# Optimization experiments

Measured on AMD Instinct MI355X. Metric: run time of the kernel, lower is better.

Reference implementation:

```python
import jax, jax.numpy as jnp
import numpy as np

GROUPS = 32
GN_EPS = 1e-6


def setup_inputs() -> dict:
    key = jax.random.key(0)
    ks = jax.random.split(key, 6)
    B, C, H, W = 2, 512, 64, 64
    s = 1.0 / np.sqrt(C)
    return {
        "x": jax.random.normal(ks[0], (B, C, H, W), jnp.float32),
        "gamma": jnp.ones((C,), jnp.float32),
        "beta": jnp.zeros((C,), jnp.float32),
        "wq": jax.random.normal(ks[1], (C, C), jnp.float32) * s,
        "bq": jnp.zeros((C,), jnp.float32),
        "wk": jax.random.normal(ks[2], (C, C), jnp.float32) * s,
        "bk": jnp.zeros((C,), jnp.float32),
        "wv": jax.random.normal(ks[3], (C, C), jnp.float32) * s,
        "bv": jnp.zeros((C,), jnp.float32),
        "wp": jax.random.normal(ks[4], (C, C), jnp.float32) * s,
        "bp": jnp.zeros((C,), jnp.float32),
    }


def _group_norm(x, gamma, beta):
    B, C, H, W = x.shape
    xg = x.reshape(B, GROUPS, C // GROUPS, H, W)
    mean = jnp.mean(xg, axis=(2, 3, 4), keepdims=True)
    var = jnp.mean(jnp.square(xg - mean), axis=(2, 3, 4), keepdims=True)
    xn = ((xg - mean) * jax.lax.rsqrt(var + GN_EPS)).reshape(B, C, H, W)
    return xn * gamma[None, :, None, None] + beta[None, :, None, None]


def _conv1x1(x, w, b):
    # 1x1 conv == per-pixel linear over channels; w: [out, in]
    return jnp.einsum('oc,bchw->bohw', w, x) + b[None, :, None, None]


def reference(x, gamma, beta, wq, bq, wk, bk, wv, bv, wp, bp):
    B, C, H, W = x.shape
    N = H * W
    h = _group_norm(x, gamma, beta)
    q = _conv1x1(h, wq, bq).reshape(B, C, N)  # [B, C, N]
    k = _conv1x1(h, wk, bk).reshape(B, C, N)
    v = _conv1x1(h, wv, bv).reshape(B, C, N)
    scale = C ** (-0.5)
    # attn[b, i, j] = softmax_j(q_i . k_j * scale)
    scores = jnp.einsum('bci,bcj->bij', q, k) * scale
    attn = jax.nn.softmax(scores, axis=2)
    # out[b, c, i] = sum_j attn[b, i, j] * v[b, c, j]
    o = jnp.einsum('bij,bcj->bci', attn, v).reshape(B, C, H, W)
    o = _conv1x1(o, wp, bp)
    return x + o
```

## Files before the change

### kernel.cpp

```cpp
#include <hip/hip_runtime.h>
#include <hip/hip_bf16.h>

using bf16 = __hip_bfloat16;
typedef __attribute__((ext_vector_type(4))) float f32x4;
typedef __attribute__((ext_vector_type(8))) short bf16x8;

#define NPX 4096
#define CCH 512

struct Ptr8 { void* p[8]; };

struct GemmP {
  const bf16* A; const bf16* B; void* C;
  const float* bias_m; const float* bias_n; const float* resid;
  float* rspart;
  float alpha; int K;
  int lda, ldb, ldc;
  long long sA, sB, sC, sR;
  int gx, gy;
  int omode;
};

__device__ __forceinline__ void async16(const bf16* g, bf16* l) {
  __builtin_amdgcn_global_load_lds((const __attribute__((address_space(1))) void*)g,
                                   (__attribute__((address_space(3))) void*)l, 16, 0, 0);
}

__device__ __forceinline__ float bfb2f(short s) {
  unsigned u = ((unsigned)(unsigned short)s) << 16;
  float f;
  __builtin_memcpy(&f, &u, 4);
  return f;
}

__device__ __forceinline__ short f2bfb(float f) {
  bf16 h = __float2bfloat16(f);
  short s;
  __builtin_memcpy(&s, &h, 2);
  return s;
}

__global__ __launch_bounds__(256) void prep_kernel(
    const float* __restrict__ wq, const float* __restrict__ wk,
    const float* __restrict__ wv, const float* __restrict__ wp,
    const float* __restrict__ bq, const float* __restrict__ bk,
    const float* __restrict__ x,
    bf16* __restrict__ wout, float* __restrict__ bqk, float* __restrict__ pstats) {
  int bid = blockIdx.x;
  int t = threadIdx.x;
  if (bid < 1024) {
    int tid = bid * 256 + t;
    int i = tid * 4;
    int seg = i >> 18;
    const float* in = seg == 0 ? wq : seg == 1 ? wk : seg == 2 ? wv : wp;
    float4 v = *reinterpret_cast<const float4*>(in + (i & 262143));
    wout[i]     = __float2bfloat16(v.x);
    wout[i + 1] = __float2bfloat16(v.y);
    wout[i + 2] = __float2bfloat16(v.z);
    wout[i + 3] = __float2bfloat16(v.w);
    if (tid < 256) {
      int j = tid * 4;
      const float* bsrc = j < 512 ? bq : bk;
      float4 b = *reinterpret_cast<const float4*>(bsrc + (j & 511));
      *reinterpret_cast<float4*>(bqk + j) = b;
    }
  } else {
    int bp = bid - 1024;
    const float* p = x + (size_t)bp * 8192;
    float s = 0.f, s2 = 0.f;
    #pragma unroll
    for (int j = 0; j < 8; j++) {
      float4 v = *reinterpret_cast<const float4*>(p + j * 1024 + t * 4);
      s  += v.x + v.y + v.z + v.w;
      s2 += v.x * v.x + v.y * v.y + v.z * v.z + v.w * v.w;
    }
    #pragma unroll
    for (int off = 32; off >= 1; off >>= 1) {
      s  += __shfl_xor(s, off);
      s2 += __shfl_xor(s2, off);
    }
    __shared__ float ls[8];
    int wv_ = t >> 6;
    if ((t & 63) == 0) { ls[wv_ * 2] = s; ls[wv_ * 2 + 1] = s2; }
    __syncthreads();
    if (t == 0) {
      pstats[bp * 2]     = ls[0] + ls[2] + ls[4] + ls[6];
      pstats[bp * 2 + 1] = ls[1] + ls[3] + ls[5] + ls[7];
    }
  }
}

__global__ __launch_bounds__(256) void gn_apply_kernel(const float* __restrict__ x,
    const float* __restrict__ pstats, const float* __restrict__ gamma,
    const float* __restrict__ beta, bf16* __restrict__ h) {
  __shared__ float tile[64][65];
  __shared__ float mr[4][2];
  int b  = blockIdx.z;
  int c0 = blockIdx.x * 64, n0 = blockIdx.y * 64;
  int t  = threadIdx.x;
  if (t < 4) {
    int g = (c0 >> 4) + t;
    float S = 0.f, S2 = 0.f;
    #pragma unroll
    for (int k2 = 0; k2 < 8; k2++) {
      S  += pstats[((b * 32 + g) * 8 + k2) * 2];
      S2 += pstats[((b * 32 + g) * 8 + k2) * 2 + 1];
    }
    float mean = S * (1.f / 65536.f);
    float var  = S2 * (1.f / 65536.f) - mean * mean;
    mr[t][0] = mean;
    mr[t][1] = rsqrtf(var + 1e-6f);
  }
  __syncthreads();
  int cl = t >> 6, nl = t & 63;
  #pragma unroll
  for (int i = 0; i < 16; i++) {
    int c = c0 + cl + i * 4;
    float v = x[((size_t)b * CCH + c) * NPX + n0 + nl];
    int gi = (cl + i * 4) >> 4;
    tile[cl + i * 4][nl] = (v - mr[gi][0]) * mr[gi][1] * gamma[c] + beta[c];
  }
  __syncthreads();
  #pragma unroll
  for (int i = 0; i < 16; i++) {
    int n = cl + i * 4;
    int c = nl;
    h[((size_t)b * NPX + n0 + n) * CCH + c0 + c] = __float2bfloat16(tile[c][n]);
  }
}

__global__ __launch_bounds__(256, 4) void gemm_any_kernel(GemmP p0, GemmP p1, unsigned nb0) {
  unsigned nwg = gridDim.x;
  unsigned flat = blockIdx.x;
  unsigned swz = (flat & 7) * (nwg >> 3) + (flat >> 3);
  GemmP p = swz < nb0 ? p0 : p1;
  unsigned local = swz < nb0 ? swz : swz - nb0;
  unsigned bxi = local % p.gx;
  unsigned tmp = local / p.gx;
  unsigned byi = tmp % p.gy;
  unsigned bz  = tmp / p.gy;

  const bf16* A = p.A + (size_t)bz * p.sA;
  const bf16* B = p.B + (size_t)bz * p.sB;
  const int m0 = bxi * 128, n0 = byi * 128;

  __shared__ bf16 ldsA[128 * 64];
  __shared__ bf16 ldsB[128 * 64];

  const int t = threadIdx.x;
  const int lane = t & 63, wv = t >> 6;
  const int wr = (wv >> 1) * 64, wc = (wv & 1) * 64;

  const int r0 = t >> 3;
  const int cb = ((t & 7) << 4) ^ ((r0 & 7) << 4);
  const bf16* gA = A + (size_t)(m0 + r0) * p.lda + (cb >> 1);
  const bf16* gB = B + (size_t)(n0 + r0) * p.ldb + (cb >> 1);
  bf16* lA = ldsA + t * 8;
  bf16* lB = ldsB + t * 8;

  const int arow = wr + (lane & 15);
  const int brow = wc + (lane & 15);
  const int kb   = (lane >> 4) * 16;

  f32x4 acc[4][4] = {};

  for (int k0 = 0; k0 < p.K; k0 += 64) {
    #pragma unroll
    for (int i = 0; i < 4; i++) {
      async16(gA + (size_t)i * 32 * p.lda + k0, lA + i * 2048);
      async16(gB + (size_t)i * 32 * p.ldb + k0, lB + i * 2048);
    }
    __syncthreads();
    #pragma unroll
    for (int ks = 0; ks < 2; ks++) {
      bf16x8 af[4], bfr[4];
      #pragma unroll
      for (int f = 0; f < 4; f++) {
        int ra = arow + f * 16;
        af[f] = *reinterpret_cast<const bf16x8*>(
            reinterpret_cast<const char*>(ldsA) + ra * 128 + ((ks * 64 + kb) ^ ((ra & 7) << 4)));
        int rb = brow + f * 16;
        bfr[f] = *reinterpret_cast<const bf16x8*>(
            reinterpret_cast<const char*>(ldsB) + rb * 128 + ((ks * 64 + kb) ^ ((rb & 7) << 4)));
      }
      #pragma unroll
      for (int fm = 0; fm < 4; fm++)
        #pragma unroll
        for (int fn = 0; fn < 4; fn++)
          acc[fm][fn] = __builtin_amdgcn_mfma_f32_16x16x32_bf16(af[fm], bfr[fn], acc[fm][fn], 0, 0, 0);
    }
    __syncthreads();
  }

  #pragma unroll
  for (int fm = 0; fm < 4; fm++) {
    #pragma unroll
    for (int j = 0; j < 4; j++) {
      int gm = m0 + wr + fm * 16 + (lane >> 4) * 4 + j;
      if (p.omode == 2) {
        float rsum = 0.f;
        #pragma unroll
        for (int fn = 0; fn < 4; fn++) {
          int gn = n0 + wc + fn * 16 + (lane & 15);
          float e = __expf(acc[fm][fn][j] * p.alpha);
          rsum += e;
          reinterpret_cast<bf16*>(p.C)[(size_t)bz * p.sC + (size_t)gm * p.ldc + gn] = __float2bfloat16(e);
        }
        rsum += __shfl_xor(rsum, 1);
        rsum += __shfl_xor(rsum, 2);
        rsum += __shfl_xor(rsum, 4);
        rsum += __shfl_xor(rsum, 8);
        if ((lane & 15) == 0)
          p.rspart[(((size_t)bz * 4096 + gm) << 6) + byi * 2 + (wv & 1)] = rsum;
      } else {
        float bm = p.bias_m ? p.bias_m[gm] : 0.f;
        #pragma unroll
        for (int fn = 0; fn < 4; fn++) {
          int gn = n0 + wc + fn * 16 + (lane & 15);
          float vv = acc[fm][fn][j] * p.alpha + bm;
          if (p.bias_n) vv += p.bias_n[gn];
          if (p.resid)  vv += p.resid[(size_t)bz * p.sR + (size_t)gm * p.ldc + gn];
          if (p.omode == 1)
            reinterpret_cast<bf16*>(p.C)[(size_t)bz * p.sC + (size_t)gm * p.ldc + gn] = __float2bfloat16(vv);
          else
            reinterpret_cast<float*>(p.C)[(size_t)bz * p.sC + (size_t)gm * p.ldc + gn] = vv;
        }
      }
    }
  }
}

#define BAR() __builtin_amdgcn_s_barrier()
#define LGKM0() do { asm volatile("s_waitcnt lgkmcnt(0)" ::: "memory"); \
                     __builtin_amdgcn_sched_barrier(0); } while (0)
#define VMC2() do { asm volatile("s_waitcnt vmcnt(2)" ::: "memory"); \
                    __builtin_amdgcn_sched_barrier(0); } while (0)
#define VMC0() do { asm volatile("s_waitcnt vmcnt(0)" ::: "memory"); \
                    __builtin_amdgcn_sched_barrier(0); } while (0)

#define STG(op, buf, half, kt, LD) do { \
    const bf16* _s = (op ? gB : gA) + (size_t)((half) * 128) * (LD) + (kt) * 64; \
    bf16* _d = &lds[op][buf][half][t * 8]; \
    async16(_s, _d); \
    async16(_s + (size_t)64 * (LD), _d + 4096); \
  } while (0)

#define DSA(buf, mrb) do { \
    _Pragma("unroll") \
    for (int mi = 0; mi < 4; mi++) { \
      int _r = ((mrb) + mi) * 16 + (l & 15); \
      _Pragma("unroll") \
      for (int ks = 0; ks < 2; ks++) \
        aR[mi][ks] = *reinterpret_cast<const bf16x8*>( \
            &lds[0][buf][wm][_r * 64 + ((ks * 32 + (l >> 4) * 8) ^ ((l & 7) << 3))]); \
    } } while (0)

#define DSB(buf, nrb) do { \
    _Pragma("unroll") \
    for (int ni = 0; ni < 2; ni++) { \
      int _r = (wn & 1) * 64 + ((nrb) + ni) * 16 + (l & 15); \
      _Pragma("unroll") \
      for (int ks = 0; ks < 2; ks++) \
        bR[ni][ks] = *reinterpret_cast<const bf16x8*>( \
            &lds[1][buf][wn >> 1][_r * 64 + ((ks * 32 + (l >> 4) * 8) ^ ((l & 7) << 3))]); \
    } } while (0)

#define MMAQ(qm, qn) do { \
    _Pragma("unroll") \
    for (int mi = 0; mi < 4; mi++) \
    _Pragma("unroll") \
    for (int ni = 0; ni < 2; ni++) \
    _Pragma("unroll") \
    for (int ks = 0; ks < 2; ks++) \
      acc[(qm) * 4 + mi][(qn) * 2 + ni] = __builtin_amdgcn_mfma_f32_16x16x32_bf16( \
          aR[mi][ks], bR[ni][ks], acc[(qm) * 4 + mi][(qn) * 2 + ni], 0, 0, 0); \
  } while (0)

#define PH_TAIL(qm, qn) do { \
    BAR(); LGKM0(); \
    __builtin_amdgcn_s_setprio(1); MMAQ(qm, qn); __builtin_amdgcn_s_setprio(0); \
    BAR(); } while (0)

__global__ __launch_bounds__(512, 1) void pv8_kernel(
    const bf16* __restrict__ Sb, const bf16* __restrict__ vb,
    const float* __restrict__ rspart, Ptr8 slots) {
  unsigned nwg = gridDim.x;
  unsigned flat = blockIdx.x;
  unsigned swz = (flat & 7) * (nwg >> 3) + (flat >> 3);
  const unsigned zz = swz >> 5;
  const unsigned tile = swz & 31;
  const int m0 = (tile & 15) * 256;
  const int n0 = (tile >> 4) * 256;
  const int b = zz >> 2, s = zz & 3;
  const bf16* A = Sb + (size_t)b * 16777216 + s * 1024;
  const bf16* B = vb + (size_t)b * 2097152 + s * 1024;
  bf16* Cp = (bf16*)(slots.p[zz]);

  __shared__ bf16 lds[2][2][2][8192];
  __shared__ float rs_lds[256];

  const int t = threadIdx.x;
  const int l = t & 63;
  const int wid = t >> 6;
  const int wm = wid >> 2;
  const int wn = wid & 3;

  const int swzc = (((t & 7) ^ ((t >> 3) & 7)) << 3);
  const bf16* gA = A + (size_t)(m0 + (t >> 3)) * 4096 + swzc;
  const bf16* gB = B + (size_t)(n0 + (t >> 3)) * 4096 + swzc;

  f32x4 acc[8][4] = {};
  bf16x8 aR[4][2], bR[2][2];

  STG(0, 0, 0, 0, 4096);
  STG(0, 0, 1, 0, 4096);
  STG(1, 0, 0, 0, 4096);
  STG(1, 0, 1, 0, 4096);
  STG(1, 1, 0, 1, 4096);
  VMC0();
  BAR();

  #pragma unroll 1
  for (int j = 0; j < 7; j++) {
    const int kt1 = 2 * j + 1, kt2 = 2 * j + 2, kt3 = 2 * j + 3;
    DSA(0, 0); DSB(0, 0); STG(1, 1, 1, kt1, 4096); PH_TAIL(0, 0);
    DSA(0, 4);            STG(0, 1, 0, kt1, 4096); PH_TAIL(1, 0);
    DSB(0, 2);            STG(0, 1, 1, kt1, 4096); PH_TAIL(1, 1);
    DSA(0, 0);            STG(1, 0, 0, kt2, 4096); VMC2(); PH_TAIL(0, 1);
    DSA(1, 0); DSB(1, 0); STG(1, 0, 1, kt2, 4096); PH_TAIL(0, 0);
    DSA(1, 4);            STG(0, 0, 0, kt2, 4096); PH_TAIL(1, 0);
    DSB(1, 2);            STG(0, 0, 1, kt2, 4096); PH_TAIL(1, 1);
    DSA(1, 0);            STG(1, 1, 0, kt3, 4096); VMC2(); PH_TAIL(0, 1);
  }
  {
    const int kt1 = 15;
    DSA(0, 0); DSB(0, 0); STG(1, 1, 1, kt1, 4096); PH_TAIL(0, 0);
    DSA(0, 4);            STG(0, 1, 0, kt1, 4096); PH_TAIL(1, 0);
    DSB(0, 2);            STG(0, 1, 1, kt1, 4096); PH_TAIL(1, 1);
    DSA(0, 0);            VMC0(); PH_TAIL(0, 1);
    DSA(1, 0); DSB(1, 0); PH_TAIL(0, 0);
    DSA(1, 4);            PH_TAIL(1, 0);
    DSB(1, 2);            PH_TAIL(1, 1);
    DSA(1, 0);            PH_TAIL(0, 1);
  }

  if (t < 256) {
    const float4* pp = reinterpret_cast<const float4*>(
        rspart + (((size_t)b * 4096 + m0 + t) << 6));
    float ssum = 0.f;
    #pragma unroll
    for (int i2 = 0; i2 < 16; i2++) {
      float4 vv = pp[i2];
      ssum += vv.x + vv.y + vv.z + vv.w;
    }
    rs_lds[t] = 1.0f / ssum;
  }
  __syncthreads();

  #pragma unroll
  for (int mr = 0; mr < 8; mr++) {
    #pragma unroll
    for (int jj = 0; jj < 4; jj++) {
      int lrow = wm * 128 + mr * 16 + (l >> 4) * 4 + jj;
      float inv = rs_lds[lrow];
      int gm = m0 + lrow;
      #pragma unroll
      for (int nr = 0; nr < 4; nr++) {
        int gn = n0 + wn * 64 + nr * 16 + (l & 15);
        Cp[(size_t)gm * 512 + gn] = __float2bfloat16(acc[mr][nr][jj] * inv);
      }
    }
  }
}

__global__ __launch_bounds__(512, 1) void qk8_kernel(
    const bf16* __restrict__ qkb, bf16* __restrict__ Sb,
    float* __restrict__ rspart, float scale) {
  unsigned nwg = gridDim.x;
  unsigned flat = blockIdx.x;
  unsigned swz = (flat & 7) * (nwg >> 3) + (flat >> 3);
  const unsigned b = swz >> 8;
  const unsigned tile = swz & 255;
  const int m0 = (tile & 15) * 256;
  const int n0 = (tile >> 4) * 256;
  const bf16* A = qkb + (size_t)b * 4194304;
  const bf16* B = qkb + (size_t)b * 4194304 + 512;
  bf16* Cp = Sb + (size_t)b * 16777216;

  __shared__ bf16 lds[2][2][2][8192];

  const int t = threadIdx.x;
  const int l = t & 63;
  const int wid = t >> 6;
  const int wm = wid >> 2;
  const int wn = wid & 3;

  const int swzc = (((t & 7) ^ ((t >> 3) & 7)) << 3);
  const bf16* gA = A + (size_t)(m0 + (t >> 3)) * 1024 + swzc;
  const bf16* gB = B + (size_t)(n0 + (t >> 3)) * 1024 + swzc;

  f32x4 acc[8][4] = {};
  bf16x8 aR[4][2], bR[2][2];

  STG(0, 0, 0, 0, 1024);
  STG(0, 0, 1, 0, 1024);
  STG(1, 0, 0, 0, 1024);
  STG(1, 0, 1, 0, 1024);
  STG(1, 1, 0, 1, 1024);
  VMC0();
  BAR();

  #pragma unroll 1
  for (int j = 0; j < 3; j++) {
    const int kt1 = 2 * j + 1, kt2 = 2 * j + 2, kt3 = 2 * j + 3;
    DSA(0, 0); DSB(0, 0); STG(1, 1, 1, kt1, 1024); PH_TAIL(0, 0);
    DSA(0, 4);            STG(0, 1, 0, kt1, 1024); PH_TAIL(1, 0);
    DSB(0, 2);            STG(0, 1, 1, kt1, 1024); PH_TAIL(1, 1);
    DSA(0, 0);            STG(1, 0, 0, kt2, 1024); VMC2(); PH_TAIL(0, 1);
    DSA(1, 0); DSB(1, 0); STG(1, 0, 1, kt2, 1024); PH_TAIL(0, 0);
    DSA(1, 4);            STG(0, 0, 0, kt2, 1024); PH_TAIL(1, 0);
    DSB(1, 2);            STG(0, 0, 1, kt2, 1024); PH_TAIL(1, 1);
    DSA(1, 0);            STG(1, 1, 0, kt3, 1024); VMC2(); PH_TAIL(0, 1);
  }
  {
    const int kt1 = 7;
    DSA(0, 0); DSB(0, 0); STG(1, 1, 1, kt1, 1024); PH_TAIL(0, 0);
    DSA(0, 4);            STG(0, 1, 0, kt1, 1024); PH_TAIL(1, 0);
    DSB(0, 2);            STG(0, 1, 1, kt1, 1024); PH_TAIL(1, 1);
    DSA(0, 0);            VMC0(); PH_TAIL(0, 1);
    DSA(1, 0); DSB(1, 0); PH_TAIL(0, 0);
    DSA(1, 4);            PH_TAIL(1, 0);
    DSB(1, 2);            PH_TAIL(1, 1);
    DSA(1, 0);            PH_TAIL(0, 1);
  }

  const int ntile = tile >> 4;
  #pragma unroll
  for (int mr = 0; mr < 8; mr++) {
    #pragma unroll
    for (int jj = 0; jj < 4; jj++) {
      int gm = m0 + wm * 128 + mr * 16 + (l >> 4) * 4 + jj;
      float rsum = 0.f;
      #pragma unroll
      for (int nr = 0; nr < 4; nr++) {
        int gn = n0 + wn * 64 + nr * 16 + (l & 15);
        float e = __expf(acc[mr][nr][jj] * scale);
        rsum += e;
        Cp[(size_t)gm * 4096 + gn] = __float2bfloat16(e);
      }
      rsum += __shfl_xor(rsum, 1);
      rsum += __shfl_xor(rsum, 2);
      rsum += __shfl_xor(rsum, 4);
      rsum += __shfl_xor(rsum, 8);
      if ((l & 15) == 0)
        rspart[(((size_t)b * 4096 + gm) << 6) + ntile * 4 + wn] = rsum;
    }
  }
}

__global__ __launch_bounds__(256, 4) void pv_split_kernel(
    const bf16* __restrict__ Sb, const bf16* __restrict__ vb,
    const float* __restrict__ rspart,
    long long sS, long long sV, Ptr8 slots, int mode) {
  unsigned nx = gridDim.x, ny = gridDim.y;
  unsigned flat = (blockIdx.z * ny + blockIdx.y) * nx + blockIdx.x;
  unsigned nwg = nx * ny * gridDim.z;
  unsigned swz = (flat & 7) * (nwg >> 3) + (flat >> 3);
  unsigned bxi = swz % nx;
  unsigned tmp = swz / nx;
  unsigned byi = tmp % ny;
  unsigned bz  = tmp / ny;

  const int z = bz;
  const int b = mode ? 0 : (z >> 2);
  const int s = mode ? z : (z & 3);
  const bf16* A = Sb + (size_t)b * sS + s * 1024;
  const bf16* B = vb + (size_t)b * sV + s * 1024;
  bf16* Cp = (bf16*)(slots.p[z]);
  const int m0 = bxi * 128, n0 = byi * 128;

  __shared__ bf16 ldsA[128 * 64];
  __shared__ bf16 ldsB[128 * 64];
  __shared__ float rs_lds[128];

  const int t = threadIdx.x;

  if (t < 128) {
    const float4* pp = reinterpret_cast<const float4*>(rspart + (((size_t)b * 4096 + m0 + t) << 6));
    float ssum = 0.f;
    #pragma unroll
    for (int i2 = 0; i2 < 16; i2++) {
      float4 vv = pp[i2];
      ssum += vv.x + vv.y + vv.z + vv.w;
    }
    rs_lds[t] = 1.0f / ssum;
  }

  const int lane = t & 63, wv = t >> 6;
  const int wr = (wv >> 1) * 64, wc = (wv & 1) * 64;

  const int r0 = t >> 3;
  const int cb = ((t & 7) << 4) ^ ((r0 & 7) << 4);
  const bf16* gA = A + (size_t)(m0 + r0) * 4096 + (cb >> 1);
  const bf16* gB = B + (size_t)(n0 + r0) * 4096 + (cb >> 1);
  bf16* lA = ldsA + t * 8;
  bf16* lB = ldsB + t * 8;

  const int arow = wr + (lane & 15);
  const int brow = wc + (lane & 15);
  const int kb   = (lane >> 4) * 16;

  f32x4 acc[4][4] = {};

  for (int k0 = 0; k0 < 1024; k0 += 64) {
    #pragma unroll
    for (int i = 0; i < 4; i++) {
      async16(gA + (size_t)i * 32 * 4096 + k0, lA + i * 2048);
      async16(gB + (size_t)i * 32 * 4096 + k0, lB + i * 2048);
    }
    __syncthreads();
    #pragma unroll
    for (int ks = 0; ks < 2; ks++) {
      bf16x8 af[4], bfr[4];
      #pragma unroll
      for (int f = 0; f < 4; f++) {
        int ra = arow + f * 16;
        af[f] = *reinterpret_cast<const bf16x8*>(
            reinterpret_cast<const char*>(ldsA) + ra * 128 + ((ks * 64 + kb) ^ ((ra & 7) << 4)));
        int rb = brow + f * 16;
        bfr[f] = *reinterpret_cast<const bf16x8*>(
            reinterpret_cast<const char*>(ldsB) + rb * 128 + ((ks * 64 + kb) ^ ((rb & 7) << 4)));
      }
      #pragma unroll
      for (int fm = 0; fm < 4; fm++)
        #pragma unroll
        for (int fn = 0; fn < 4; fn++)
          acc[fm][fn] = __builtin_amdgcn_mfma_f32_16x16x32_bf16(af[fm], bfr[fn], acc[fm][fn], 0, 0, 0);
    }
    __syncthreads();
  }

  #pragma unroll
  for (int fm = 0; fm < 4; fm++) {
    #pragma unroll
    for (int j = 0; j < 4; j++) {
      int lrow = wr + fm * 16 + (lane >> 4) * 4 + j;
      float inv = rs_lds[lrow];
      int gm = m0 + lrow;
      #pragma unroll
      for (int fn = 0; fn < 4; fn++) {
        int gn = n0 + wc + fn * 16 + (lane & 15);
        Cp[(size_t)gm * 512 + gn] = __float2bfloat16(acc[fm][fn][j] * inv);
      }
    }
  }
}

__global__ __launch_bounds__(256) void reduce3x2_kernel(bf16* __restrict__ o,
    const bf16* __restrict__ h, const bf16* __restrict__ qk) {
  int i = (blockIdx.x * 256 + threadIdx.x) * 8;
  int b = i >> 21;
  int ii = i & 2097151;
  bf16* dst = o + (size_t)b * 2097152 + ii;
  const bf16* p1 = h + (size_t)b * 2097152 + ii;
  const bf16* p2 = qk + (size_t)b * 2 * 2097152 + ii;
  const bf16* p3 = qk + (size_t)(b * 2 + 1) * 2097152 + ii;
  bf16x8 a  = *reinterpret_cast<const bf16x8*>(dst);
  bf16x8 v1 = *reinterpret_cast<const bf16x8*>(p1);
  bf16x8 v2 = *reinterpret_cast<const bf16x8*>(p2);
  bf16x8 v3 = *reinterpret_cast<const bf16x8*>(p3);
  bf16x8 r;
  #pragma unroll
  for (int j = 0; j < 8; j++)
    r[j] = f2bfb(bfb2f(a[j]) + bfb2f(v1[j]) + bfb2f(v2[j]) + bfb2f(v3[j]));
  *reinterpret_cast<bf16x8*>(dst) = r;
}

__global__ __launch_bounds__(256) void reduce3_kernel(bf16* __restrict__ dst,
    const bf16* __restrict__ p1, const bf16* __restrict__ p2,
    const bf16* __restrict__ p3) {
  int i = (blockIdx.x * 256 + threadIdx.x) * 8;
  bf16x8 a  = *reinterpret_cast<const bf16x8*>(dst + i);
  bf16x8 v1 = *reinterpret_cast<const bf16x8*>(p1 + i);
  bf16x8 v2 = *reinterpret_cast<const bf16x8*>(p2 + i);
  bf16x8 v3 = *reinterpret_cast<const bf16x8*>(p3 + i);
  bf16x8 r;
  #pragma unroll
  for (int j = 0; j < 8; j++)
    r[j] = f2bfb(bfb2f(a[j]) + bfb2f(v1[j]) + bfb2f(v2[j]) + bfb2f(v3[j]));
  *reinterpret_cast<bf16x8*>(dst + i) = r;
}

extern "C" void kernel_launch(void* const* d_in, const int* in_sizes, int n_in,
                              void* d_out, int out_size, void* d_ws, size_t ws_size,
                              hipStream_t stream) {
  const float* x     = (const float*)d_in[0];
  const float* gamma = (const float*)d_in[1];
  const float* beta  = (const float*)d_in[2];
  const float* wq    = (const float*)d_in[3];
  const float* bq    = (const float*)d_in[4];
  const float* wk    = (const float*)d_in[5];
  const float* bk    = (const float*)d_in[6];
  const float* wv    = (const float*)d_in[7];
  const float* bv    = (const float*)d_in[8];
  const float* wp    = (const float*)d_in[9];
  const float* bp    = (const float*)d_in[10];
  float* out = (float*)d_out;

  char* w = (char*)d_ws;
  size_t off = 0;
  float* pstats = (float*)(w + off);   off += 4096;
  float* bqk    = (float*)(w + off);   off += 4096;
  float* rspart = (float*)(w + off);   off += (size_t)2 * 4096 * 64 * 4;
  bf16* wqkb = (bf16*)(w + off);       off += (size_t)1024 * 512 * 2;
  bf16* wvb  = (bf16*)(w + off);       off += (size_t)512 * 512 * 2;
  bf16* wpb  = (bf16*)(w + off);       off += (size_t)512 * 512 * 2;
  bf16* h    = (bf16*)(w + off);       off += (size_t)2 * NPX * CCH * 2;
  bf16* qk   = (bf16*)(w + off);       off += (size_t)2 * NPX * 1024 * 2;
  bf16* v    = (bf16*)(w + off);       off += (size_t)2 * NPX * CCH * 2;
  bf16* o    = (bf16*)(w + off);       off += (size_t)2 * NPX * CCH * 2;
  bf16* S    = (bf16*)(w + off);
  size_t need_big = off + (size_t)2 * NPX * NPX * 2;
  const bool big = ws_size >= need_big;

  const long long sBN = (long long)NPX * CCH;
  const long long sQK = (long long)NPX * 1024;
  const long long sS  = (long long)NPX * NPX;
  const float scale = 0.04419417382415922f;

  prep_kernel<<<1536, 256, 0, stream>>>(wq, wk, wv, wp, bq, bk, x, wqkb, bqk, pstats);
  gn_apply_kernel<<<dim3(8, 64, 2), 256, 0, stream>>>(x, pstats, gamma, beta, h);

  GemmP pqkv = {h, wqkb, qk, nullptr, bqk, nullptr, nullptr,
                1.f, 512, 512, 512, 1024, sBN, 0, sQK, 0, 32, 8, 1};
  GemmP pv   = {wvb, h, v, bv, nullptr, nullptr, nullptr,
                1.f, 512, 512, 512, 4096, 0, sBN, sBN, 0, 4, 32, 1};
  gemm_any_kernel<<<768, 256, 0, stream>>>(pqkv, pv, 512);

  if (big) {
    qk8_kernel<<<512, 512, 0, stream>>>(qk, S, rspart, scale);
    Ptr8 slots{{o, h, qk, qk + sBN, o + sBN, h + sBN, qk + 2 * sBN, qk + 3 * sBN}};
    pv8_kernel<<<256, 512, 0, stream>>>(S, v, rspart, slots);
    reduce3x2_kernel<<<2048, 256, 0, stream>>>(o, h, qk);
  } else {
    for (int b = 0; b < 2; b++) {
      GemmP ps = {qk + b * sQK, qk + b * sQK + 512, S, nullptr, nullptr, nullptr,
                  rspart + ((size_t)b << 18),
                  scale, 512, 1024, 1024, 4096, 0, 0, 0, 0, 32, 32, 2};
      gemm_any_kernel<<<1024, 256, 0, stream>>>(ps, ps, 1024);
      Ptr8 slots{{o + b * sBN, h, h + sBN, (bf16*)out, nullptr, nullptr, nullptr, nullptr}};
      pv_split_kernel<<<dim3(32, 4, 4), 256, 0, stream>>>(S, v + b * sBN,
          rspart + ((size_t)b << 18), 0, 0, slots, 1);
      reduce3_kernel<<<1024, 256, 0, stream>>>(o + b * sBN, h, h + sBN, (bf16*)out);
    }
  }

  GemmP po = {wpb, o, out, bp, nullptr, x, nullptr,
              1.f, 512, 512, 512, 4096, 0, sBN, sBN, sBN, 4, 32, 0};
  gemm_any_kernel<<<256, 256, 0, stream>>>(po, po, 256);
}
```

Baseline: 246.3 us.

## Process both batches per workgroup in QK kernel with mid-loop epilogue

```diff
diff --git a/kernel.cpp b/kernel.cpp
--- a/kernel.cpp
+++ b/kernel.cpp
@@ -220,7 +220,7 @@
           float vv = acc[fm][fn][j] * p.alpha + bm;
           if (p.bias_n) vv += p.bias_n[gn];
           if (p.resid)  vv += p.resid[(size_t)bz * p.sR + (size_t)gm * p.ldc + gn];
-          if (p.omode == 1)
+        if (p.omode == 1)
             reinterpret_cast<bf16*>(p.C)[(size_t)bz * p.sC + (size_t)gm * p.ldc + gn] = __float2bfloat16(vv);
           else
             reinterpret_cast<float*>(p.C)[(size_t)bz * p.sC + (size_t)gm * p.ldc + gn] = vv;
@@ -243,6 +243,15 @@
     bf16* _d = &lds[op][buf][half][t * 8]; \
     async16(_s, _d); \
     async16(_s + (size_t)64 * (LD), _d + 4096); \
+  } while (0)
+
+#define STGQ(op, buf, half, kt) do { \
+    int _k = (kt); \
+    const bf16* _base = (op) ? (_k < 8 ? gB0 : gB1) : (_k < 8 ? gA0 : gA1); \
+    const bf16* _s = _base + (size_t)((half) * 128) * 1024 + (_k & 7) * 64; \
+    bf16* _d = &lds[op][buf][half][t * 8]; \
+    async16(_s, _d); \
+    async16(_s + (size_t)64 * 1024, _d + 4096); \
   } while (0)
 
 #define DSA(buf, mrb) do { \
@@ -379,13 +388,9 @@
   unsigned nwg = gridDim.x;
   unsigned flat = blockIdx.x;
   unsigned swz = (flat & 7) * (nwg >> 3) + (flat >> 3);
-  const unsigned b = swz >> 8;
   const unsigned tile = swz & 255;
   const int m0 = (tile & 15) * 256;
   const int n0 = (tile >> 4) * 256;
-  const bf16* A = qkb + (size_t)b * 4194304;
-  const bf16* B = qkb + (size_t)b * 4194304 + 512;
-  bf16* Cp = Sb + (size_t)b * 16777216;
 
   __shared__ bf16 lds[2][2][2][8192];
 
@@ -396,66 +401,80 @@
   const int wn = wid & 3;
 
   const int swzc = (((t & 7) ^ ((t >> 3) & 7)) << 3);
-  const bf16* gA = A + (size_t)(m0 + (t >> 3)) * 1024 + swzc;
-  const bf16* gB = B + (size_t)(n0 + (t >> 3)) * 1024 + swzc;
+  const bf16* gA0 = qkb + (size_t)(m0 + (t >> 3)) * 1024 + swzc;
+  const bf16* gB0 = qkb + 512 + (size_t)(n0 + (t >> 3)) * 1024 + swzc;
+  const bf16* gA1 = gA0 + 4194304;
+  const bf16* gB1 = gB0 + 4194304;
 
   f32x4 acc[8][4] = {};
   bf16x8 aR[4][2], bR[2][2];
 
-  STG(0, 0, 0, 0, 1024);
-  STG(0, 0, 1, 0, 1024);
-  STG(1, 0, 0, 0, 1024);
-  STG(1, 0, 1, 0, 1024);
-  STG(1, 1, 0, 1, 1024);
+  auto epi = [&](int b) {
+    const int ntile = tile >> 4;
+    bf16* Cp = Sb + (size_t)b * 16777216;
+    #pragma unroll
+    for (int mr = 0; mr < 8; mr++) {
+      #pragma unroll
+      for (int jj = 0; jj < 4; jj++) {
+        int gm = m0 + wm * 128 + mr * 16 + (l >> 4) * 4 + jj;
+        float rsum = 0.f;
+        #pragma unroll
+        for (int nr = 0; nr < 4; nr++) {
+          int gn = n0 + wn * 64 + nr * 16 + (l & 15);
+          float e = __expf(acc[mr][nr][jj] * scale);
+          rsum += e;
+          Cp[(size_t)gm * 4096 + gn] = __float2bfloat16(e);
+        }
+        rsum += __shfl_xor(rsum, 1);
+        rsum += __shfl_xor(rsum, 2);
+        rsum += __shfl_xor(rsum, 4);
+        rsum += __shfl_xor(rsum, 8);
+        if ((l & 15) == 0)
+          rspart[(((size_t)b * 4096 + gm) << 6) + ntile * 4 + wn] = rsum;
+      }
+    }
+  };
+
+  STGQ(0, 0, 0, 0);
+  STGQ(0, 0, 1, 0);
+  STGQ(1, 0, 0, 0);
+  STGQ(1, 0, 1, 0);
+  STGQ(1, 1, 0, 1);
   VMC0();
   BAR();
 
   #pragma unroll 1
-  for (int j = 0; j < 3; j++) {
+  for (int j = 0; j < 7; j++) {
     const int kt1 = 2 * j + 1, kt2 = 2 * j + 2, kt3 = 2 * j + 3;
-    DSA(0, 0); DSB(0, 0); STG(1, 1, 1, kt1, 1024); PH_TAIL(0, 0);
-    DSA(0, 4);            STG(0, 1, 0, kt1, 1024); PH_TAIL(1, 0);
-    DSB(0, 2);            STG(0, 1, 1, kt1, 1024); PH_TAIL(1, 1);
-    DSA(0, 0);            STG(1, 0, 0, kt2, 1024); VMC2(); PH_TAIL(0, 1);
-    DSA(1, 0); DSB(1, 0); STG(1, 0, 1, kt2, 1024); PH_TAIL(0, 0);
-    DSA(1, 4);            STG(0, 0, 0, kt2, 1024); PH_TAIL(1, 0);
-    DSB(1, 2);            STG(0, 0, 1, kt2, 1024); PH_TAIL(1, 1);
-    DSA(1, 0);            STG(1, 1, 0, kt3, 1024); VMC2(); PH_TAIL(0, 1);
+    DSA(0, 0); DSB(0, 0); STGQ(1, 1, 1, kt1); PH_TAIL(0, 0);
+    DSA(0, 4);            STGQ(0, 1, 0, kt1); PH_TAIL(1, 0);
+    DSB(0, 2);            STGQ(0, 1, 1, kt1); PH_TAIL(1, 1);
+    DSA(0, 0);            STGQ(1, 0, 0, kt2); VMC2(); PH_TAIL(0, 1);
+    DSA(1, 0); DSB(1, 0); STGQ(1, 0, 1, kt2); PH_TAIL(0, 0);
+    DSA(1, 4);            STGQ(0, 0, 0, kt2); PH_TAIL(1, 0);
+    DSB(1, 2);            STGQ(0, 0, 1, kt2); PH_TAIL(1, 1);
+    DSA(1, 0);            STGQ(1, 1, 0, kt3); VMC2(); PH_TAIL(0, 1);
+    if (j == 3) {
+      epi(0);
+      #pragma unroll
+      for (int a1 = 0; a1 < 8; a1++)
+        #pragma unroll
+        for (int a2 = 0; a2 < 4; a2++)
+          acc[a1][a2] = f32x4{0.f, 0.f, 0.f, 0.f};
+    }
   }
   {
-    const int kt1 = 7;
-    DSA(0, 0); DSB(0, 0); STG(1, 1, 1, kt1, 1024); PH_TAIL(0, 0);
-    DSA(0, 4);            STG(0, 1, 0, kt1, 1024); PH_TAIL(1, 0);
-    DSB(0, 2);            STG(0, 1, 1, kt1, 1024); PH_TAIL(1, 1);
+    const int kt1 = 15;
+    DSA(0, 0); DSB(0, 0); STGQ(1, 1, 1, kt1); PH_TAIL(0, 0);
+    DSA(0, 4);            STGQ(0, 1, 0, kt1); PH_TAIL(1, 0);
+    DSB(0, 2);            STGQ(0, 1, 1, kt1); PH_TAIL(1, 1);
     DSA(0, 0);            VMC0(); PH_TAIL(0, 1);
     DSA(1, 0); DSB(1, 0); PH_TAIL(0, 0);
     DSA(1, 4);            PH_TAIL(1, 0);
     DSB(1, 2);            PH_TAIL(1, 1);
     DSA(1, 0);            PH_TAIL(0, 1);
   }
-
-  const int ntile = tile >> 4;
-  #pragma unroll
-  for (int mr = 0; mr < 8; mr++) {
-    #pragma unroll
-    for (int jj = 0; jj < 4; jj++) {
-      int gm = m0 + wm * 128 + mr * 16 + (l >> 4) * 4 + jj;
-      float rsum = 0.f;
-      #pragma unroll
-      for (int nr = 0; nr < 4; nr++) {
-        int gn = n0 + wn * 64 + nr * 16 + (l & 15);
-        float e = __expf(acc[mr][nr][jj] * scale);
-        rsum += e;
-        Cp[(size_t)gm * 4096 + gn] = __float2bfloat16(e);
-      }
-      rsum += __shfl_xor(rsum, 1);
-      rsum += __shfl_xor(rsum, 2);
-      rsum += __shfl_xor(rsum, 4);
-      rsum += __shfl_xor(rsum, 8);
-      if ((l & 15) == 0)
-        rspart[(((size_t)b * 4096 + gm) << 6) + ntile * 4 + wn] = rsum;
-    }
-  }
+  epi(1);
 }
 
 __global__ __launch_bounds__(256, 4) void pv_split_kernel(
@@ -638,7 +657,7 @@
   gemm_any_kernel<<<768, 256, 0, stream>>>(pqkv, pv, 512);
 
   if (big) {
-    qk8_kernel<<<512, 512, 0, stream>>>(qk, S, rspart, scale);
+    qk8_kernel<<<256, 512, 0, stream>>>(qk, S, rspart, scale);
     Ptr8 slots{{o, h, qk, qk + sBN, o + sBN, h + sBN, qk + 2 * sBN, qk + 3 * sBN}};
     pv8_kernel<<<256, 512, 0, stream>>>(S, v, rspart, slots);
     reduce3x2_kernel<<<2048, 256, 0, stream>>>(o, h, qk);
```

Result: slower. 371.2 us (+50.7%).

## Fuse split-K partial reduction into output projection GEMM B-tile loading

Applied to the files above, without the earlier changes.

```diff
diff --git a/kernel.cpp b/kernel.cpp
--- a/kernel.cpp
+++ b/kernel.cpp
@@ -230,6 +230,100 @@
   }
 }
 
+__global__ __launch_bounds__(256, 4) void outproj_kernel(
+    const bf16* __restrict__ A, const bf16* __restrict__ B1b,
+    const bf16* __restrict__ hb, const bf16* __restrict__ qkb,
+    const float* __restrict__ bp, const float* __restrict__ x,
+    float* __restrict__ out) {
+  unsigned nwg = gridDim.x;
+  unsigned flat = blockIdx.x;
+  unsigned swz = (flat & 7) * (nwg >> 3) + (flat >> 3);
+  unsigned bxi = swz % 4;
+  unsigned tmp = swz / 4;
+  unsigned byi = tmp % 32;
+  unsigned bz  = tmp / 32;
+
+  const long long sBN = (long long)NPX * CCH;
+  const bf16* B1 = B1b + (size_t)bz * sBN;
+  const bf16* B2 = hb  + (size_t)bz * sBN;
+  const bf16* B3 = qkb + (size_t)bz * 2 * sBN;
+  const bf16* B4 = qkb + sBN + (size_t)bz * 2 * sBN;
+  const int m0 = bxi * 128, n0 = byi * 128;
+
+  __shared__ bf16 ldsA[128 * 64];
+  __shared__ bf16 ldsB[128 * 64];
+
+  const int t = threadIdx.x;
+  const int lane = t & 63, wv = t >> 6;
+  const int wr = (wv >> 1) * 64, wc = (wv & 1) * 64;
+
+  const int r0 = t >> 3;
+  const int cb = ((t & 7) << 4) ^ ((r0 & 7) << 4);
+  const bf16* gA = A + (size_t)(m0 + r0) * 512 + (cb >> 1);
+  bf16* lA = ldsA + t * 8;
+  bf16* lB = ldsB + t * 8;
+
+  const int arow = wr + (lane & 15);
+  const int brow = wc + (lane & 15);
+  const int kb   = (lane >> 4) * 16;
+
+  f32x4 acc[4][4] = {};
+
+  for (int k0 = 0; k0 < 512; k0 += 64) {
+    #pragma unroll
+    for (int i = 0; i < 4; i++)
+      async16(gA + (size_t)i * 32 * 512 + k0, lA + i * 2048);
+    #pragma unroll
+    for (int i = 0; i < 4; i++) {
+      size_t boff = (size_t)(n0 + r0 + i * 32) * 512 + (cb >> 1) + k0;
+      bf16x8 b1 = *reinterpret_cast<const bf16x8*>(B1 + boff);
+      bf16x8 b2 = *reinterpret_cast<const bf16x8*>(B2 + boff);
+      bf16x8 b3 = *reinterpret_cast<const bf16x8*>(B3 + boff);
+      bf16x8 b4 = *reinterpret_cast<const bf16x8*>(B4 + boff);
+      bf16x8 r;
+      #pragma unroll
+      for (int j = 0; j < 8; j++)
+        r[j] = f2bfb(bfb2f(b1[j]) + bfb2f(b2[j]) + bfb2f(b3[j]) + bfb2f(b4[j]));
+      *reinterpret_cast<bf16x8*>(lB + i * 2048) = r;
+    }
+    __syncthreads();
+    #pragma unroll
+    for (int ks = 0; ks < 2; ks++) {
+      bf16x8 af[4], bfr[4];
+      #pragma unroll
+      for (int f = 0; f < 4; f++) {
+        int ra = arow + f * 16;
+        af[f] = *reinterpret_cast<const bf16x8*>(
+            reinterpret_cast<const char*>(ldsA) + ra * 128 + ((ks * 64 + kb) ^ ((ra & 7) << 4)));
+        int rb = brow + f * 16;
+        bfr[f] = *reinterpret_cast<const bf16x8*>(
+            reinterpret_cast<const char*>(ldsB) + rb * 128 + ((ks * 64 + kb) ^ ((rb & 7) << 4)));
+      }
+      #pragma unroll
+      for (int fm = 0; fm < 4; fm++)
+        #pragma unroll
+        for (int fn = 0; fn < 4; fn++)
+          acc[fm][fn] = __builtin_amdgcn_mfma_f32_16x16x32_bf16(af[fm], bfr[fn], acc[fm][fn], 0, 0, 0);
+    }
+    __syncthreads();
+  }
+
+  #pragma unroll
+  for (int fm = 0; fm < 4; fm++) {
+    #pragma unroll
+    for (int j = 0; j < 4; j++) {
+      int gm = m0 + wr + fm * 16 + (lane >> 4) * 4 + j;
+      float bm = bp[gm];
+      #pragma unroll
+      for (int fn = 0; fn < 4; fn++) {
+        int gn = n0 + wc + fn * 16 + (lane & 15);
+        size_t co = (size_t)bz * 2097152 + (size_t)gm * 4096 + gn;
+        out[co] = acc[fm][fn][j] + bm + x[co];
+      }
+    }
+  }
+}
+
 #define BAR() __builtin_amdgcn_s_barrier()
 #define LGKM0() do { asm volatile("s_waitcnt lgkmcnt(0)" ::: "memory"); \
                      __builtin_amdgcn_sched_barrier(0); } while (0)
@@ -554,26 +648,6 @@
       }
     }
   }
-}
-
-__global__ __launch_bounds__(256) void reduce3x2_kernel(bf16* __restrict__ o,
-    const bf16* __restrict__ h, const bf16* __restrict__ qk) {
-  int i = (blockIdx.x * 256 + threadIdx.x) * 8;
-  int b = i >> 21;
-  int ii = i & 2097151;
-  bf16* dst = o + (size_t)b * 2097152 + ii;
-  const bf16* p1 = h + (size_t)b * 2097152 + ii;
-  const bf16* p2 = qk + (size_t)b * 2 * 2097152 + ii;
-  const bf16* p3 = qk + (size_t)(b * 2 + 1) * 2097152 + ii;
-  bf16x8 a  = *reinterpret_cast<const bf16x8*>(dst);
-  bf16x8 v1 = *reinterpret_cast<const bf16x8*>(p1);
-  bf16x8 v2 = *reinterpret_cast<const bf16x8*>(p2);
-  bf16x8 v3 = *reinterpret_cast<const bf16x8*>(p3);
-  bf16x8 r;
-  #pragma unroll
-  for (int j = 0; j < 8; j++)
-    r[j] = f2bfb(bfb2f(a[j]) + bfb2f(v1[j]) + bfb2f(v2[j]) + bfb2f(v3[j]));
-  *reinterpret_cast<bf16x8*>(dst) = r;
 }
 
 __global__ __launch_bounds__(256) void reduce3_kernel(bf16* __restrict__ dst,
@@ -641,7 +715,7 @@
     qk8_kernel<<<512, 512, 0, stream>>>(qk, S, rspart, scale);
     Ptr8 slots{{o, h, qk, qk + sBN, o + sBN, h + sBN, qk + 2 * sBN, qk + 3 * sBN}};
     pv8_kernel<<<256, 512, 0, stream>>>(S, v, rspart, slots);
-    reduce3x2_kernel<<<2048, 256, 0, stream>>>(o, h, qk);
+    outproj_kernel<<<256, 256, 0, stream>>>(wpb, o, h, qk, bp, x, out);
   } else {
     for (int b = 0; b < 2; b++) {
       GemmP ps = {qk + b * sQK, qk + b * sQK + 512, S, nullptr, nullptr, nullptr,
@@ -653,9 +727,8 @@
           rspart + ((size_t)b << 18), 0, 0, slots, 1);
       reduce3_kernel<<<1024, 256, 0, stream>>>(o + b * sBN, h, h + sBN, (bf16*)out);
     }
-  }
-
-  GemmP po = {wpb, o, out, bp, nullptr, x, nullptr,
-              1.f, 512, 512, 512, 4096, 0, sBN, sBN, sBN, 4, 32, 0};
-  gemm_any_kernel<<<256, 256, 0, stream>>>(po, po, 256);
-}
+    GemmP po = {wpb, o, out, bp, nullptr, x, nullptr,
+                1.f, 512, 512, 512, 4096, 0, sBN, sBN, sBN, 4, 32, 0};
+    gemm_any_kernel<<<256, 256, 0, stream>>>(po, po, 256);
+  }
+}
```

Result: no change. 245.5 us (-0.3%).
